# Kernel tuning notes

Measured on AMD Instinct MI355X. Metric: run time of the kernel, lower is better.

## Reference

```python
import jax, jax.numpy as jnp
import numpy as np

EPS = 1.0 / 137.0
OUT_FEATURES = 8192

def setup_inputs() -> dict:
    key = jax.random.key(0)
    k1, k2 = jax.random.split(key)
    x = jax.random.normal(k1, (8, 2048, 2048), dtype=jnp.float32)
    # lecun_normal-like scale for kernel
    kernel = jax.random.normal(k2, (2048, OUT_FEATURES), dtype=jnp.float32) * (1.0 / np.sqrt(2048))
    bias = jnp.zeros((OUT_FEATURES,), dtype=jnp.float32)
    alpha = jnp.ones((1,), dtype=jnp.float32)
    return {"x": x, "kernel": kernel, "bias": bias, "alpha": alpha}

def reference(x, kernel, bias, alpha):
    # y = x @ kernel : [B, S, out]
    y = jnp.einsum("bsd,do->bso", x, kernel)
    x_sq = jnp.sum(x * x, axis=-1, keepdims=True)            # [B, S, 1]
    k_sq = jnp.sum(kernel * kernel, axis=0, keepdims=True)   # [1, out]
    distances = x_sq + k_sq - 2.0 * y                         # ||x - w||^2
    y = (y * y) / (distances + EPS)
    y = y + bias.reshape((1,) * (y.ndim - 1) + (-1,))
    scale = (jnp.sqrt(jnp.float32(OUT_FEATURES)) / jnp.log1p(jnp.float32(OUT_FEATURES))) ** alpha
    return y * scale
```

## Files before the change

### kernel.cpp

```cpp
#include <hip/hip_runtime.h>
#include <hip/hip_bf16.h>
#include <math.h>


#define EPS_F (1.0f / 137.0f)
#define M_DIM 16384
#define N_DIM 8192
#define K_DIM 2048

typedef __attribute__((ext_vector_type(8))) short short8;
typedef __attribute__((ext_vector_type(4))) float f32x4;

__device__ __forceinline__ unsigned short f2bf(float f) {
  unsigned int u = __float_as_uint(f);
  u += 0x7fffu + ((u >> 16) & 1u);
  return (unsigned short)(u >> 16);
}

typedef __attribute__((address_space(1))) const unsigned int as1_cuint;
typedef __attribute__((address_space(3))) unsigned int as3_uint;

__device__ __forceinline__ void gload16(const void* g, void* lds_wave_base) {
  __builtin_amdgcn_global_load_lds((as1_cuint*)g, (as3_uint*)lds_wave_base, 16, 0, 0);
}


__global__ __launch_bounds__(256) void k_conv_x(const float* __restrict__ x,
                                                unsigned short* __restrict__ xbf,
                                                float* __restrict__ xs) {
  const int row = blockIdx.x;
  const int t = threadIdx.x;
  const float4* xr = (const float4*)(x + (size_t)row * K_DIM);
  ushort4* orow = (ushort4*)(xbf + (size_t)row * K_DIM);
  float s = 0.f;
#pragma unroll
  for (int i = 0; i < 2; ++i) {
    float4 v = xr[t + i * 256];
    s += v.x * v.x + v.y * v.y + v.z * v.z + v.w * v.w;
    ushort4 o;
    o.x = f2bf(v.x); o.y = f2bf(v.y); o.z = f2bf(v.z); o.w = f2bf(v.w);
    orow[t + i * 256] = o;
  }
#pragma unroll
  for (int off = 32; off > 0; off >>= 1) s += __shfl_down(s, off, 64);
  __shared__ float red[4];
  if ((t & 63) == 0) red[t >> 6] = s;
  __syncthreads();
  if (t == 0) xs[row] = red[0] + red[1] + red[2] + red[3];
}

__global__ __launch_bounds__(256) void k_conv_kT_fused(const float* __restrict__ w,
                                                       unsigned short* __restrict__ bt,
                                                       float* __restrict__ kpart) {
  __shared__ float tile[32][33];
  __shared__ float psum[8][33];
  const int tx = threadIdx.x;
  const int ty = threadIdx.y;
  const int n0 = blockIdx.x * 32;
  const int k0 = blockIdx.y * 32;
  float ss = 0.f;
#pragma unroll
  for (int j = 0; j < 32; j += 8) {
    float v = w[(size_t)(k0 + ty + j) * N_DIM + n0 + tx];
    tile[ty + j][tx] = v;
    ss += v * v;
  }
  psum[ty][tx] = ss;
  __syncthreads();
#pragma unroll
  for (int j = 0; j < 32; j += 8)
    bt[(size_t)(n0 + ty + j) * K_DIM + k0 + tx] = f2bf(tile[tx][ty + j]);
  if (ty == 0) {
    float s = 0.f;
#pragma unroll
    for (int r = 0; r < 8; ++r) s += psum[r][tx];
    kpart[(size_t)(k0 >> 5) * N_DIM + n0 + tx] = s;
  }
}

__global__ __launch_bounds__(256) void k_conv_kT(const float* __restrict__ w,
                                                 unsigned short* __restrict__ bt) {
  __shared__ float tile[32][33];
  const int tx = threadIdx.x;
  const int ty = threadIdx.y;
  const int n0 = blockIdx.x * 32;
  const int k0 = blockIdx.y * 32;
#pragma unroll
  for (int j = 0; j < 32; j += 8)
    tile[ty + j][tx] = w[(size_t)(k0 + ty + j) * N_DIM + n0 + tx];
  __syncthreads();
#pragma unroll
  for (int j = 0; j < 32; j += 8)
    bt[(size_t)(n0 + ty + j) * K_DIM + k0 + tx] = f2bf(tile[tx][ty + j]);
}

__global__ __launch_bounds__(256) void k_ksq_part(const float* __restrict__ w,
                                                  float* __restrict__ kpart) {
  const int col = blockIdx.x * 256 + threadIdx.x;
  const int kb = blockIdx.y;
  float s = 0.f;
#pragma unroll 4
  for (int k = kb * 128; k < kb * 128 + 128; ++k) {
    float v = w[(size_t)k * N_DIM + col];
    s += v * v;
  }
  kpart[kb * N_DIM + col] = s;
}

__global__ __launch_bounds__(256) void k_ksq_fin(const float* __restrict__ kpart,
                                                 float* __restrict__ ks, int nkb) {
  const int col = blockIdx.x * 256 + threadIdx.x;
  float s = 0.f;
  for (int kb = 0; kb < nkb; ++kb) s += kpart[(size_t)kb * N_DIM + col];
  ks[col] = s;
}


#define MFMA_OP(d, va, vb) \
  d = __builtin_amdgcn_mfma_f32_16x16x32_bf16(va, vb, d, 0, 0, 0)

#define FENCE asm volatile("" ::: "memory")
#define BAR do { FENCE; __builtin_amdgcn_s_barrier(); FENCE; } while (0)
#define VMCNT6  asm volatile("s_waitcnt vmcnt(6)" ::: "memory")
#define VMCNT12 asm volatile("s_waitcnt vmcnt(12)" ::: "memory")

__global__ __launch_bounds__(512, 2) void k_gemm(const unsigned short* __restrict__ A,
                                                 const unsigned short* __restrict__ B,
                                                 const float* __restrict__ xs,
                                                 const float* __restrict__ ks,
                                                 const float* __restrict__ bias,
                                                 const float* __restrict__ alpha,
                                                 float* __restrict__ out) {
  __shared__ __align__(16) char lds[147456];
  char* sA = lds;
  char* sB = lds + 98304;

  const int t = threadIdx.x;
  const int lane = t & 63;
  const int wid = t >> 6;
  const int wr = wid >> 1;
  const int wc = wid & 1;
  const int lr = lane & 15;
  const int kh = lane >> 4;
  const int swz = (lr & 7) << 4;

  const int bid = blockIdx.x;
  const int xcd = bid & 7;
  const int sub = bid >> 3;
  const int ch  = sub >> 5;
  const int w32 = sub & 31;
  const int tm = ((xcd >> 1) << 4) + ((ch >> 2) << 2) + (w32 >> 3);
  const int tn = ((xcd & 1) << 5) + ((ch & 3) << 3) + (w32 & 7);
  const size_t rowM0 = (size_t)tm * 256;
  const size_t colN0 = (size_t)tn * 128;

  const int l8 = lane >> 3;
  const int col16 = (lane & 7) ^ (l8 & 7);
  const unsigned short* gA0 = A + (rowM0 + wid * 8 + l8) * K_DIM + col16 * 8;
  const unsigned short* gB0 = B + (colN0 + wid * 8 + l8) * K_DIM + col16 * 8;

#define STAGE_A(boff, s, ko) \
  gload16(gA0 + (size_t)(s) * 64 * K_DIM + (ko), \
          sA + (boff) + ((s) * 64 + wid * 8) * 128)
#define STAGE_B(boff, j, ko) \
  gload16(gB0 + (size_t)(j) * 64 * K_DIM + (ko), \
          sB + (boff) + ((j) * 64 + wid * 8) * 128)

#define RD_A(boff, m, kk) \
  (*(const short8*)(sA + (boff) + (wr * 64 + (m) * 16 + lr) * 128 + \
                    (((kk) * 64 + kh * 16) ^ swz)))
#define RD_B(boff, n, kk) \
  (*(const short8*)(sB + (boff) + (wc * 64 + (n) * 16 + lr) * 128 + \
                    (((kk) * 64 + kh * 16) ^ swz)))

  f32x4 acc[4][4] = {};
  short8 aX[8], bX[8], aY[8], bY[8];

#define LOAD_A8(AS, boff) do { \
  AS[0] = RD_A(boff, 0, 0); AS[1] = RD_A(boff, 0, 1); \
  AS[2] = RD_A(boff, 1, 0); AS[3] = RD_A(boff, 1, 1); \
  AS[4] = RD_A(boff, 2, 0); AS[5] = RD_A(boff, 2, 1); \
  AS[6] = RD_A(boff, 3, 0); AS[7] = RD_A(boff, 3, 1); \
} while (0)
#define LOAD_B8(BS, boff) do { \
  BS[0] = RD_B(boff, 0, 0); BS[1] = RD_B(boff, 0, 1); \
  BS[2] = RD_B(boff, 1, 0); BS[3] = RD_B(boff, 1, 1); \
  BS[4] = RD_B(boff, 2, 0); BS[5] = RD_B(boff, 2, 1); \
  BS[6] = RD_B(boff, 3, 0); BS[7] = RD_B(boff, 3, 1); \
} while (0)

#define MFMA16(mb, AS, BS) do { \
  __builtin_amdgcn_s_setprio(1); \
  MFMA_OP(acc[mb][0], AS[(mb)*2], BS[0]); MFMA_OP(acc[mb][1], AS[(mb)*2], BS[2]); \
  MFMA_OP(acc[mb][2], AS[(mb)*2], BS[4]); MFMA_OP(acc[mb][3], AS[(mb)*2], BS[6]); \
  MFMA_OP(acc[(mb)+1][0], AS[(mb)*2+2], BS[0]); MFMA_OP(acc[(mb)+1][1], AS[(mb)*2+2], BS[2]); \
  MFMA_OP(acc[(mb)+1][2], AS[(mb)*2+2], BS[4]); MFMA_OP(acc[(mb)+1][3], AS[(mb)*2+2], BS[6]); \
  MFMA_OP(acc[mb][0], AS[(mb)*2+1], BS[1]); MFMA_OP(acc[mb][1], AS[(mb)*2+1], BS[3]); \
  MFMA_OP(acc[mb][2], AS[(mb)*2+1], BS[5]); MFMA_OP(acc[mb][3], AS[(mb)*2+1], BS[7]); \
  MFMA_OP(acc[(mb)+1][0], AS[(mb)*2+3], BS[1]); MFMA_OP(acc[(mb)+1][1], AS[(mb)*2+3], BS[3]); \
  MFMA_OP(acc[(mb)+1][2], AS[(mb)*2+3], BS[5]); MFMA_OP(acc[(mb)+1][3], AS[(mb)*2+3], BS[7]); \
  __builtin_amdgcn_s_setprio(0); \
} while (0)

  STAGE_A(0, 0, 0); STAGE_A(0, 1, 0); STAGE_A(0, 2, 0); STAGE_A(0, 3, 0);
  STAGE_B(0, 0, 0); STAGE_B(0, 1, 0);
  STAGE_A(32768, 0, 64); STAGE_A(32768, 1, 64); STAGE_A(32768, 2, 64); STAGE_A(32768, 3, 64);
  STAGE_B(16384, 0, 64); STAGE_B(16384, 1, 64);
  STAGE_A(65536, 0, 128); STAGE_A(65536, 1, 128); STAGE_A(65536, 2, 128); STAGE_A(65536, 3, 128);
  STAGE_B(32768, 0, 128); STAGE_B(32768, 1, 128);
  VMCNT12;
  BAR;
  LOAD_B8(bX, 0);
  LOAD_A8(aX, 0);
  VMCNT6;
  BAR;

  int cA0 = 0, cA1 = 32768, cA2 = 65536;
  int cB0 = 0, cB1 = 16384, cB2 = 32768;

#pragma unroll 1
  for (int it = 0; it < 16; ++it) {
    const int koE = (it <= 14) ? (2 * it + 3) * 64 : 0;
    const int koO = (it <= 13) ? (2 * it + 4) * 64 : 0;
    LOAD_B8(bY, cB1);
    STAGE_A(cA0, 0, koE); STAGE_A(cA0, 1, koE); STAGE_A(cA0, 2, koE);
    BAR; MFMA16(0, aX, bX); BAR;
    LOAD_A8(aY, cA1);
    STAGE_A(cA0, 3, koE); STAGE_B(cB0, 0, koE); STAGE_B(cB0, 1, koE);
    BAR; MFMA16(2, aX, bX); VMCNT6; BAR;
    LOAD_B8(bX, cB2);
    STAGE_A(cA1, 0, koO); STAGE_A(cA1, 1, koO); STAGE_A(cA1, 2, koO);
    BAR; MFMA16(0, aY, bY); BAR;
    LOAD_A8(aX, cA2);
    STAGE_A(cA1, 3, koO); STAGE_B(cB1, 0, koO); STAGE_B(cB1, 1, koO);
    BAR; MFMA16(2, aY, bY); VMCNT6; BAR;
    int tA = cA2; cA2 = cA1; cA1 = cA0; cA0 = tA;
    int tB = cB2; cB2 = cB1; cB1 = cB0; cB0 = tB;
  }

  asm volatile("s_waitcnt vmcnt(0)" ::: "memory");

  const float scale = powf(sqrtf(8192.0f) / log1pf(8192.0f), alpha[0]);
#pragma unroll
  for (int m = 0; m < 4; ++m) {
#pragma unroll
    for (int r = 0; r < 4; ++r) {
      const size_t grow = rowM0 + wr * 64 + m * 16 + kh * 4 + r;
      const float xq = xs[grow];
      float* orow = out + grow * N_DIM;
#pragma unroll
      for (int n = 0; n < 4; ++n) {
        const int gcol = (int)colN0 + wc * 64 + n * 16 + lr;
        const float y = acc[m][n][r];
        const float d = xq + ks[gcol] - 2.0f * y + EPS_F;
        const float v = y * y * __builtin_amdgcn_rcpf(d);
        orow[gcol] = (v + bias[gcol]) * scale;
      }
    }
  }
}


extern "C" void kernel_launch(void* const* d_in, const int* in_sizes, int n_in,
                              void* d_out, int out_size, void* d_ws, size_t ws_size,
                              hipStream_t stream) {
  const float* x     = (const float*)d_in[0];
  const float* w     = (const float*)d_in[1];
  const float* bias  = (const float*)d_in[2];
  const float* alpha = (const float*)d_in[3];
  float* out = (float*)d_out;
  char* ws = (char*)d_ws;

  unsigned short* xbf = (unsigned short*)(ws);
  unsigned short* ktb = (unsigned short*)(ws + 67108864);
  float* xs    = (float*)(ws + 100663296);
  float* ks    = (float*)(ws + 100728832);
  float* kpart = (float*)(ws + 100761600);

  k_conv_x<<<M_DIM, 256, 0, stream>>>(x, xbf, xs);
  if (ws_size >= 100761600ull + (size_t)64 * N_DIM * 4) {
    k_conv_kT_fused<<<dim3(N_DIM / 32, K_DIM / 32), dim3(32, 8), 0, stream>>>(w, ktb, kpart);
    k_ksq_fin<<<N_DIM / 256, 256, 0, stream>>>(kpart, ks, 64);
  } else {
    k_conv_kT<<<dim3(N_DIM / 32, K_DIM / 32), dim3(32, 8), 0, stream>>>(w, ktb);
    k_ksq_part<<<dim3(N_DIM / 256, 16), 256, 0, stream>>>(w, kpart);
    k_ksq_fin<<<N_DIM / 256, 256, 0, stream>>>(kpart, ks, 16);
  }
  k_gemm<<<(M_DIM / 256) * (N_DIM / 128), 512, 0, stream>>>(xbf, ktb, xs, ks, bias, alpha, out);
}
```

Before: 659.6 us.

## Restructure GEMM main loop to 32-wide K tiles with triple-buffered smaller LDS

The bf16 GEMM now steps K in chunks of 32 instead of 64, with a three-stage LDS ring of 72KB. It uses a new 4-slot XOR swizzle and a simplified per-tile load/barrier/MFMA sequence. Launch bounds now target four blocks per CU instead of two, and the block-to-tile mapping is changed. The conversion kernels also switch to nontemporal loads. Higher occupancy is meant to hide latency, but it costs more barriers per unit of K, a shallower per-wave register prefetch, and tighter register budgets.

```diff
diff --git a/kernel.cpp b/kernel.cpp
--- a/kernel.cpp
+++ b/kernel.cpp
@@ -30,12 +30,12 @@
                                                 float* __restrict__ xs) {
   const int row = blockIdx.x;
   const int t = threadIdx.x;
-  const float4* xr = (const float4*)(x + (size_t)row * K_DIM);
+  const f32x4* xr = (const f32x4*)(x + (size_t)row * K_DIM);
   ushort4* orow = (ushort4*)(xbf + (size_t)row * K_DIM);
   float s = 0.f;
 #pragma unroll
   for (int i = 0; i < 2; ++i) {
-    float4 v = xr[t + i * 256];
+    f32x4 v = __builtin_nontemporal_load(&xr[t + i * 256]);
     s += v.x * v.x + v.y * v.y + v.z * v.z + v.w * v.w;
     ushort4 o;
     o.x = f2bf(v.x); o.y = f2bf(v.y); o.z = f2bf(v.z); o.w = f2bf(v.w);
@@ -61,7 +61,7 @@
   float ss = 0.f;
 #pragma unroll
   for (int j = 0; j < 32; j += 8) {
-    float v = w[(size_t)(k0 + ty + j) * N_DIM + n0 + tx];
+    float v = __builtin_nontemporal_load(&w[(size_t)(k0 + ty + j) * N_DIM + n0 + tx]);
     tile[ty + j][tx] = v;
     ss += v * v;
   }
@@ -87,7 +87,7 @@
   const int k0 = blockIdx.y * 32;
 #pragma unroll
   for (int j = 0; j < 32; j += 8)
-    tile[ty + j][tx] = w[(size_t)(k0 + ty + j) * N_DIM + n0 + tx];
+    tile[ty + j][tx] = __builtin_nontemporal_load(&w[(size_t)(k0 + ty + j) * N_DIM + n0 + tx]);
   __syncthreads();
 #pragma unroll
   for (int j = 0; j < 32; j += 8)
@@ -119,21 +119,23 @@
 #define MFMA_OP(d, va, vb) \
   d = __builtin_amdgcn_mfma_f32_16x16x32_bf16(va, vb, d, 0, 0, 0)
 
-#define FENCE asm volatile("" ::: "memory")
-#define BAR do { FENCE; __builtin_amdgcn_s_barrier(); FENCE; } while (0)
-#define VMCNT6  asm volatile("s_waitcnt vmcnt(6)" ::: "memory")
-#define VMCNT12 asm volatile("s_waitcnt vmcnt(12)" ::: "memory")
-
-__global__ __launch_bounds__(512, 2) void k_gemm(const unsigned short* __restrict__ A,
+#define BARRIER __builtin_amdgcn_s_barrier()
+#define LGKM0_SGB do { \
+  asm volatile("s_waitcnt lgkmcnt(0)" ::: "memory"); \
+  __builtin_amdgcn_sched_barrier(0); \
+} while (0)
+#define VMCNT3 asm volatile("s_waitcnt vmcnt(3)" ::: "memory")
+
+__global__ __launch_bounds__(512, 4) void k_gemm(const unsigned short* __restrict__ A,
                                                  const unsigned short* __restrict__ B,
                                                  const float* __restrict__ xs,
                                                  const float* __restrict__ ks,
                                                  const float* __restrict__ bias,
                                                  const float* __restrict__ alpha,
                                                  float* __restrict__ out) {
-  __shared__ __align__(16) char lds[147456];
+  __shared__ __align__(16) char lds[73728];
   char* sA = lds;
-  char* sB = lds + 98304;
+  char* sB = lds + 49152;
 
   const int t = threadIdx.x;
   const int lane = t & 63;
@@ -142,101 +144,78 @@
   const int wc = wid & 1;
   const int lr = lane & 15;
   const int kh = lane >> 4;
-  const int swz = (lr & 7) << 4;
+  const int rdslot = (kh ^ (lr & 3)) << 4;
 
   const int bid = blockIdx.x;
   const int xcd = bid & 7;
   const int sub = bid >> 3;
-  const int ch  = sub >> 5;
-  const int w32 = sub & 31;
-  const int tm = ((xcd >> 1) << 4) + ((ch >> 2) << 2) + (w32 >> 3);
-  const int tn = ((xcd & 1) << 5) + ((ch & 3) << 3) + (w32 & 7);
+  const int ch  = sub >> 6;
+  const int w64 = sub & 63;
+  const int tm = xcd * 8 + (w64 >> 3);
+  const int tn = ch * 8 + (w64 & 7);
   const size_t rowM0 = (size_t)tm * 256;
   const size_t colN0 = (size_t)tn * 128;
 
-  const int l8 = lane >> 3;
-  const int col16 = (lane & 7) ^ (l8 & 7);
-  const unsigned short* gA0 = A + (rowM0 + wid * 8 + l8) * K_DIM + col16 * 8;
-  const unsigned short* gB0 = B + (colN0 + wid * 8 + l8) * K_DIM + col16 * 8;
+  const int row_p = lane >> 2;
+  const int slot_p = lane & 3;
+  const int kg = slot_p ^ (row_p & 3);
+  const unsigned short* gA0 = A + (rowM0 + wid * 16 + row_p) * K_DIM + kg * 8;
+  const unsigned short* gB0 = B + (colN0 + wid * 16 + row_p) * K_DIM + kg * 8;
 
 #define STAGE_A(boff, s, ko) \
-  gload16(gA0 + (size_t)(s) * 64 * K_DIM + (ko), \
-          sA + (boff) + ((s) * 64 + wid * 8) * 128)
-#define STAGE_B(boff, j, ko) \
-  gload16(gB0 + (size_t)(j) * 64 * K_DIM + (ko), \
-          sB + (boff) + ((j) * 64 + wid * 8) * 128)
-
-#define RD_A(boff, m, kk) \
-  (*(const short8*)(sA + (boff) + (wr * 64 + (m) * 16 + lr) * 128 + \
-                    (((kk) * 64 + kh * 16) ^ swz)))
-#define RD_B(boff, n, kk) \
-  (*(const short8*)(sB + (boff) + (wc * 64 + (n) * 16 + lr) * 128 + \
-                    (((kk) * 64 + kh * 16) ^ swz)))
+  gload16(gA0 + (size_t)(s) * 128 * K_DIM + (ko), \
+          sA + (boff) + ((s) * 128 + wid * 16) * 64)
+#define STAGE_B(boff, ko) \
+  gload16(gB0 + (ko), sB + (boff) + wid * 16 * 64)
+
+#define RD_A(boff, m) \
+  (*(const short8*)(sA + (boff) + (wr * 64 + (m) * 16 + lr) * 64 + rdslot))
+#define RD_B(boff, n) \
+  (*(const short8*)(sB + (boff) + (wc * 64 + (n) * 16 + lr) * 64 + rdslot))
 
   f32x4 acc[4][4] = {};
-  short8 aX[8], bX[8], aY[8], bY[8];
-
-#define LOAD_A8(AS, boff) do { \
-  AS[0] = RD_A(boff, 0, 0); AS[1] = RD_A(boff, 0, 1); \
-  AS[2] = RD_A(boff, 1, 0); AS[3] = RD_A(boff, 1, 1); \
-  AS[4] = RD_A(boff, 2, 0); AS[5] = RD_A(boff, 2, 1); \
-  AS[6] = RD_A(boff, 3, 0); AS[7] = RD_A(boff, 3, 1); \
-} while (0)
-#define LOAD_B8(BS, boff) do { \
-  BS[0] = RD_B(boff, 0, 0); BS[1] = RD_B(boff, 0, 1); \
-  BS[2] = RD_B(boff, 1, 0); BS[3] = RD_B(boff, 1, 1); \
-  BS[4] = RD_B(boff, 2, 0); BS[5] = RD_B(boff, 2, 1); \
-  BS[6] = RD_B(boff, 3, 0); BS[7] = RD_B(boff, 3, 1); \
-} while (0)
-
-#define MFMA16(mb, AS, BS) do { \
+  short8 a[4], b[4];
+
+#define MFMA16() do { \
   __builtin_amdgcn_s_setprio(1); \
-  MFMA_OP(acc[mb][0], AS[(mb)*2], BS[0]); MFMA_OP(acc[mb][1], AS[(mb)*2], BS[2]); \
-  MFMA_OP(acc[mb][2], AS[(mb)*2], BS[4]); MFMA_OP(acc[mb][3], AS[(mb)*2], BS[6]); \
-  MFMA_OP(acc[(mb)+1][0], AS[(mb)*2+2], BS[0]); MFMA_OP(acc[(mb)+1][1], AS[(mb)*2+2], BS[2]); \
-  MFMA_OP(acc[(mb)+1][2], AS[(mb)*2+2], BS[4]); MFMA_OP(acc[(mb)+1][3], AS[(mb)*2+2], BS[6]); \
-  MFMA_OP(acc[mb][0], AS[(mb)*2+1], BS[1]); MFMA_OP(acc[mb][1], AS[(mb)*2+1], BS[3]); \
-  MFMA_OP(acc[mb][2], AS[(mb)*2+1], BS[5]); MFMA_OP(acc[mb][3], AS[(mb)*2+1], BS[7]); \
-  MFMA_OP(acc[(mb)+1][0], AS[(mb)*2+3], BS[1]); MFMA_OP(acc[(mb)+1][1], AS[(mb)*2+3], BS[3]); \
-  MFMA_OP(acc[(mb)+1][2], AS[(mb)*2+3], BS[5]); MFMA_OP(acc[(mb)+1][3], AS[(mb)*2+3], BS[7]); \
+  MFMA_OP(acc[0][0], a[0], b[0]); MFMA_OP(acc[0][1], a[0], b[1]); \
+  MFMA_OP(acc[0][2], a[0], b[2]); MFMA_OP(acc[0][3], a[0], b[3]); \
+  MFMA_OP(acc[1][0], a[1], b[0]); MFMA_OP(acc[1][1], a[1], b[1]); \
+  MFMA_OP(acc[1][2], a[1], b[2]); MFMA_OP(acc[1][3], a[1], b[3]); \
+  MFMA_OP(acc[2][0], a[2], b[0]); MFMA_OP(acc[2][1], a[2], b[1]); \
+  MFMA_OP(acc[2][2], a[2], b[2]); MFMA_OP(acc[2][3], a[2], b[3]); \
+  MFMA_OP(acc[3][0], a[3], b[0]); MFMA_OP(acc[3][1], a[3], b[1]); \
+  MFMA_OP(acc[3][2], a[3], b[2]); MFMA_OP(acc[3][3], a[3], b[3]); \
   __builtin_amdgcn_s_setprio(0); \
 } while (0)
 
-  STAGE_A(0, 0, 0); STAGE_A(0, 1, 0); STAGE_A(0, 2, 0); STAGE_A(0, 3, 0);
-  STAGE_B(0, 0, 0); STAGE_B(0, 1, 0);
-  STAGE_A(32768, 0, 64); STAGE_A(32768, 1, 64); STAGE_A(32768, 2, 64); STAGE_A(32768, 3, 64);
-  STAGE_B(16384, 0, 64); STAGE_B(16384, 1, 64);
-  STAGE_A(65536, 0, 128); STAGE_A(65536, 1, 128); STAGE_A(65536, 2, 128); STAGE_A(65536, 3, 128);
-  STAGE_B(32768, 0, 128); STAGE_B(32768, 1, 128);
-  VMCNT12;
-  BAR;
-  LOAD_B8(bX, 0);
-  LOAD_A8(aX, 0);
-  VMCNT6;
-  BAR;
-
-  int cA0 = 0, cA1 = 32768, cA2 = 65536;
-  int cB0 = 0, cB1 = 16384, cB2 = 32768;
+#define TILE32(cbA, cbB, sbA, sbB, ko) do { \
+  STAGE_A(sbA, 0, ko); STAGE_A(sbA, 1, ko); STAGE_B(sbB, ko); \
+  a[0] = RD_A(cbA, 0); a[1] = RD_A(cbA, 1); \
+  a[2] = RD_A(cbA, 2); a[3] = RD_A(cbA, 3); \
+  b[0] = RD_B(cbB, 0); b[1] = RD_B(cbB, 1); \
+  b[2] = RD_B(cbB, 2); b[3] = RD_B(cbB, 3); \
+  VMCNT3; BARRIER; LGKM0_SGB; \
+  MFMA16(); \
+  BARRIER; \
+} while (0)
+
+  STAGE_A(0, 0, 0); STAGE_A(0, 1, 0); STAGE_B(0, 0);
+  STAGE_A(16384, 0, 32); STAGE_A(16384, 1, 32); STAGE_B(8192, 32);
+  VMCNT3;
+  BARRIER;
 
 #pragma unroll 1
-  for (int it = 0; it < 16; ++it) {
-    const int koE = (it <= 14) ? (2 * it + 3) * 64 : 0;
-    const int koO = (it <= 13) ? (2 * it + 4) * 64 : 0;
-    LOAD_B8(bY, cB1);
-    STAGE_A(cA0, 0, koE); STAGE_A(cA0, 1, koE); STAGE_A(cA0, 2, koE);
-    BAR; MFMA16(0, aX, bX); BAR;
-    LOAD_A8(aY, cA1);
-    STAGE_A(cA0, 3, koE); STAGE_B(cB0, 0, koE); STAGE_B(cB0, 1, koE);
-    BAR; MFMA16(2, aX, bX); VMCNT6; BAR;
-    LOAD_B8(bX, cB2);
-    STAGE_A(cA1, 0, koO); STAGE_A(cA1, 1, koO); STAGE_A(cA1, 2, koO);
-    BAR; MFMA16(0, aY, bY); BAR;
-    LOAD_A8(aX, cA2);
-    STAGE_A(cA1, 3, koO); STAGE_B(cB1, 0, koO); STAGE_B(cB1, 1, koO);
-    BAR; MFMA16(2, aY, bY); VMCNT6; BAR;
-    int tA = cA2; cA2 = cA1; cA1 = cA0; cA0 = tA;
-    int tB = cB2; cB2 = cB1; cB1 = cB0; cB0 = tB;
-  }
+  for (int i = 0; i < 21; ++i) {
+    const int t0 = 3 * i;
+    const int ko0 = (t0 + 2) * 32;
+    const int ko1 = (t0 + 3 < 64) ? (t0 + 3) * 32 : 0;
+    const int ko2 = (t0 + 4 < 64) ? (t0 + 4) * 32 : 0;
+    TILE32(0,     0,     32768, 16384, ko0);
+    TILE32(16384, 8192,  0,     0,     ko1);
+    TILE32(32768, 16384, 16384, 8192,  ko2);
+  }
+  TILE32(0, 0, 32768, 16384, 0);
 
   asm volatile("s_waitcnt vmcnt(0)" ::: "memory");
 
```

Result: no change. 662.5 us (+0.4%).
